# Optimization experiments

Hardware: AMD Instinct MI355X
Metric: run time of the kernel (lower is better)

The kernel has to match this reference:

```python
import jax, jax.numpy as jnp
import numpy as np

NUM_HEAD = 16
HIDDEN = 1024
HEAD_DIM = HIDDEN // NUM_HEAD


def setup_inputs() -> dict:
    key = jax.random.key(0)
    k1, k2, k3, k4, k5 = jax.random.split(key, 5)
    scale = 0.02
    x = jax.random.normal(k1, (2, 2048, HIDDEN), dtype=jnp.float32)
    w_in = jax.random.normal(k2, (3 * HIDDEN, HIDDEN), dtype=jnp.float32) * scale
    b_in = jax.random.normal(k3, (3 * HIDDEN,), dtype=jnp.float32) * scale
    w_out = jax.random.normal(k4, (HIDDEN, HIDDEN), dtype=jnp.float32) * scale
    b_out = jax.random.normal(k5, (HIDDEN,), dtype=jnp.float32) * scale
    return {"x": x, "w_in": w_in, "b_in": b_in, "w_out": w_out, "b_out": b_out}


def reference(x, w_in, b_in, w_out, b_out):
    B, S, D = x.shape
    # in_proj: fused QKV, torch Linear convention y = x @ W.T + b
    qkv = x @ w_in.T + b_in                      # [B,S,3D]
    q, k, v = jnp.split(qkv, 3, axis=-1)         # each [B,S,D]
    def heads(t):
        return t.reshape(B, S, NUM_HEAD, HEAD_DIM).transpose(0, 2, 1, 3)  # [B,H,S,d]
    q, k, v = heads(q), heads(k), heads(v)
    scores = jnp.einsum("bhqd,bhkd->bhqk", q, k) / jnp.sqrt(
        jnp.asarray(HEAD_DIM, dtype=x.dtype))    # [B,H,S,S]
    attn = jax.nn.softmax(scores, axis=-1)
    out = jnp.einsum("bhqk,bhkd->bhqd", attn, v)  # [B,H,S,d]
    out = out.transpose(0, 2, 1, 3).reshape(B, S, D)
    return out @ w_out.T + b_out
```

## Files before the change

kernel.cpp:

```cpp
#include <hip/hip_runtime.h>

using u16 = unsigned short;
using u32 = unsigned int;

typedef __bf16 bf16x8 __attribute__((ext_vector_type(8)));
typedef __bf16 bf16x2 __attribute__((ext_vector_type(2)));
typedef float f32x4 __attribute__((ext_vector_type(4)));

__device__ __forceinline__ u16 f2b(float x) {
  u32 u = __builtin_bit_cast(u32, x);
  u += 0x7fffu + ((u >> 16) & 1u);
  return (u16)(u >> 16);
}

__device__ __forceinline__ u32 pk2(float lo, float hi) {
  bf16x2 t;
  t[0] = (__bf16)lo;
  t[1] = (__bf16)hi;
  return __builtin_bit_cast(u32, t);
}

__device__ __forceinline__ void gload16(const u16* g, u16* l) {
  __builtin_amdgcn_global_load_lds(
      (const __attribute__((address_space(1))) void*)g,
      (__attribute__((address_space(3))) void*)l, 16, 0, 0);
}

#define SCALE_Q 0.1803368801111204f
#define DEFER_THR 8.0f

__global__ void cvt_bf16_k(const float* __restrict__ s, u16* __restrict__ d, int n8) {
  int i = blockIdx.x * blockDim.x + threadIdx.x;
  int stride = gridDim.x * blockDim.x;
  for (; i < n8; i += stride) {
    float4 a = ((const float4*)s)[2 * i];
    float4 b = ((const float4*)s)[2 * i + 1];
    uint4 o;
    o.x = (u32)f2b(a.x) | ((u32)f2b(a.y) << 16);
    o.y = (u32)f2b(a.z) | ((u32)f2b(a.w) << 16);
    o.z = (u32)f2b(b.x) | ((u32)f2b(b.y) << 16);
    o.w = (u32)f2b(b.z) | ((u32)f2b(b.w) << 16);
    ((uint4*)d)[i] = o;
  }
}

template <int MODE, int BM>
__global__ __launch_bounds__(256) void gemm_bt(
    const u16* __restrict__ A, const u16* __restrict__ Bm,
    const float* __restrict__ bias,
    u16* __restrict__ q, u16* __restrict__ k, u16* __restrict__ v,
    float* __restrict__ outf) {
  constexpr int KD = 1024;
  constexpr int MR = BM / 32;
  const int n0 = blockIdx.x * 128;
  const int m0 = blockIdx.y * BM;
  const int tid = threadIdx.x;
  const int wid = tid >> 6;
  const int lane = tid & 63;
  const int wr = wid >> 1, wc = wid & 1;
  const int fr = lane & 15, fg = lane >> 4;
  const int srow = lane >> 2;
  const int scol = (lane & 3) * 8;

  __shared__ __align__(16) u16 As[BM * 32];
  __shared__ __align__(16) u16 Bs[128 * 32];

  f32x4 acc[MR][4] = {};

  for (int k0 = 0; k0 < KD; k0 += 32) {
#pragma unroll
    for (int i = 0; i < BM / 64; ++i) {
      int row = i * 64 + wid * 16 + srow;
      gload16(A + (size_t)(m0 + row) * KD + k0 + scol, As + (i * 64 + wid * 16) * 32);
    }
#pragma unroll
    for (int i = 0; i < 2; ++i) {
      int row = i * 64 + wid * 16 + srow;
      gload16(Bm + (size_t)(n0 + row) * KD + k0 + scol, Bs + (i * 64 + wid * 16) * 32);
    }
    __syncthreads();
    bf16x8 af[MR], bfr[4];
#pragma unroll
    for (int r = 0; r < MR; ++r)
      af[r] = *(const bf16x8*)(As + (wr * (BM / 2) + r * 16 + fr) * 32 + fg * 8);
#pragma unroll
    for (int c = 0; c < 4; ++c)
      bfr[c] = *(const bf16x8*)(Bs + (wc * 64 + c * 16 + fr) * 32 + fg * 8);
#pragma unroll
    for (int r = 0; r < MR; ++r)
#pragma unroll
      for (int c = 0; c < 4; ++c)
        acc[r][c] = __builtin_amdgcn_mfma_f32_16x16x32_bf16(af[r], bfr[c], acc[r][c], 0, 0, 0);
    __syncthreads();
  }

#pragma unroll
  for (int r = 0; r < MR; ++r) {
#pragma unroll
    for (int c = 0; c < 4; ++c) {
      const int gcol = n0 + wc * 64 + c * 16 + fr;
      const float bv = bias[gcol];
#pragma unroll
      for (int g = 0; g < 4; ++g) {
        const int grow = m0 + wr * (BM / 2) + r * 16 + fg * 4 + g;
        float val = acc[r][c][g] + bv;
        if (MODE == 0) {
          const int which = gcol >> 10;
          if (which == 0) val *= SCALE_Q;
          const int dcol = gcol & 1023;
          const int hh = dcol >> 6, dd = dcol & 63;
          const int bb = grow >> 11, ss = grow & 2047;
          u16* dst = which == 0 ? q : (which == 1 ? k : v);
          dst[((size_t)((bb << 4) + hh) * 2048 + ss) * 64 + dd] = f2b(val);
        } else {
          outf[(size_t)grow * 1024 + gcol] = val;
        }
      }
    }
  }
}

__global__ __launch_bounds__(256) void attn_fwd(
    const u16* __restrict__ Q, const u16* __restrict__ K,
    const u16* __restrict__ V, u16* __restrict__ AO) {
  const int wg = blockIdx.x;
  const int newid = (wg & 7) * 64 + (wg >> 3);
  const int bh = newid >> 4;
  const int qt = newid & 15;
  const int b = bh >> 4, h = bh & 15;

  const int tid = threadIdx.x, wid = tid >> 6, lane = tid & 63;
  const int fr = lane & 15, fg = lane >> 4;
  const size_t base = (size_t)bh * (2048 * 64);
  const int q0 = qt * 128 + wid * 32;

  constexpr int LD = 72;
  __shared__ __align__(16) u16 Ks[2][64 * LD];
  __shared__ __align__(16) u16 Vs[2][64 * LD];

  bf16x8 qf[2][2];
#pragma unroll
  for (int rf = 0; rf < 2; ++rf)
#pragma unroll
    for (int ks = 0; ks < 2; ++ks)
      qf[rf][ks] = *(const bf16x8*)(Q + base + (size_t)(q0 + rf * 16 + fr) * 64 + ks * 32 + fg * 8);

  f32x4 o[2][4] = {};
  float mrow[2] = {-3.0e38f, -3.0e38f};
  float lrow[2] = {0.f, 0.f};

  const int krow = lane;
  const int Lrow = ((krow >> 5) << 5) | (((krow >> 3) & 1) << 4) | (((krow >> 2) & 1) << 3) |
                   (((krow >> 4) & 1) << 2) | (krow & 3);
  const int c0 = wid * 16;
  const int kp2 = (lane & 31) * 2;
  const int vh = (lane >> 5) * 8;

  uint4 kr0, kr1, vr0, vr1;
  {
    const u16* kp = K + base + (size_t)Lrow * 64 + c0;
    const u16* vp = V + base + (size_t)kp2 * 64 + c0 + vh;
    kr0 = *(const uint4*)kp; kr1 = *(const uint4*)(kp + 8);
    vr0 = *(const uint4*)vp; vr1 = *(const uint4*)(vp + 64);
  }

  for (int t = 0; t < 32; ++t) {
    u16* kb = (u16*)Ks[t & 1];
    u16* vb = (u16*)Vs[t & 1];
    *(uint4*)(kb + krow * LD + c0) = kr0;
    *(uint4*)(kb + krow * LD + c0 + 8) = kr1;
    {
      const u32* ra = (const u32*)&vr0;
      const u32* rb = (const u32*)&vr1;
#pragma unroll
      for (int j = 0; j < 8; ++j) {
        u32 w = __builtin_amdgcn_perm(rb[j >> 1], ra[j >> 1],
                                      (j & 1) ? 0x07060302u : 0x05040100u);
        *(u32*)(vb + (c0 + vh + j) * LD + kp2) = w;
      }
    }
    __syncthreads();
    if (t + 1 < 32) {
      const u16* kp = K + base + (size_t)((t + 1) * 64 + Lrow) * 64 + c0;
      const u16* vp = V + base + (size_t)((t + 1) * 64 + kp2) * 64 + c0 + vh;
      kr0 = *(const uint4*)kp; kr1 = *(const uint4*)(kp + 8);
      vr0 = *(const uint4*)vp; vr1 = *(const uint4*)(vp + 64);
    }

    bf16x8 kf[4][2], vf[4][2];
#pragma unroll
    for (int c = 0; c < 4; ++c)
#pragma unroll
      for (int ks = 0; ks < 2; ++ks)
        kf[c][ks] = *(const bf16x8*)(kb + (c * 16 + fr) * LD + ks * 32 + fg * 8);
#pragma unroll
    for (int d = 0; d < 4; ++d)
#pragma unroll
      for (int ks = 0; ks < 2; ++ks)
        vf[d][ks] = *(const bf16x8*)(vb + (d * 16 + fr) * LD + ks * 32 + fg * 8);

#pragma unroll
    for (int rf = 0; rf < 2; ++rf) {
      f32x4 p[4];
      __builtin_amdgcn_s_setprio(1);
#pragma unroll
      for (int c = 0; c < 4; ++c) {
        f32x4 z = {};
        z = __builtin_amdgcn_mfma_f32_16x16x32_bf16(kf[c][0], qf[rf][0], z, 0, 0, 0);
        z = __builtin_amdgcn_mfma_f32_16x16x32_bf16(kf[c][1], qf[rf][1], z, 0, 0, 0);
        p[c] = z;
      }
      __builtin_amdgcn_s_setprio(0);
      f32x4 m4 = p[0];
#pragma unroll
      for (int c = 1; c < 4; ++c) {
        m4[0] = fmaxf(m4[0], p[c][0]); m4[1] = fmaxf(m4[1], p[c][1]);
        m4[2] = fmaxf(m4[2], p[c][2]); m4[3] = fmaxf(m4[3], p[c][3]);
      }
      float mx = fmaxf(fmaxf(m4[0], m4[1]), fmaxf(m4[2], m4[3]));
      mx = fmaxf(mx, __shfl_xor(mx, 16));
      mx = fmaxf(mx, __shfl_xor(mx, 32));

      const float mold = mrow[rf];
      const bool defer = __all(mx <= mold + DEFER_THR);
      float mnew = mold, corr = 1.0f;
      if (!defer) {
        mnew = fmaxf(mold, mx);
        corr = __builtin_amdgcn_exp2f(mold - mnew);
        mrow[rf] = mnew;
      }
      float rs = 0.f;
#pragma unroll
      for (int c = 0; c < 4; ++c)
#pragma unroll
        for (int g = 0; g < 4; ++g) {
          const float pv = __builtin_amdgcn_exp2f(p[c][g] - mnew);
          p[c][g] = pv;
          rs += pv;
        }
      rs += __shfl_xor(rs, 16);
      rs += __shfl_xor(rs, 32);
      if (defer) {
        lrow[rf] += rs;
      } else {
        lrow[rf] = lrow[rf] * corr + rs;
        float cO[4];
#pragma unroll
        for (int g = 0; g < 4; ++g) cO[g] = __shfl(corr, 20 * fg + g);
#pragma unroll
        for (int d = 0; d < 4; ++d) {
          o[rf][d][0] *= cO[0]; o[rf][d][1] *= cO[1];
          o[rf][d][2] *= cO[2]; o[rf][d][3] *= cO[3];
        }
      }

      bf16x8 pa[2];
#pragma unroll
      for (int ks = 0; ks < 2; ++ks) {
        u32 w0 = pk2(p[2 * ks][0], p[2 * ks][1]);
        u32 w1 = pk2(p[2 * ks][2], p[2 * ks][3]);
        u32 w2 = pk2(p[2 * ks + 1][0], p[2 * ks + 1][1]);
        u32 w3 = pk2(p[2 * ks + 1][2], p[2 * ks + 1][3]);
        uint4 packed = {w0, w1, w2, w3};
        pa[ks] = __builtin_bit_cast(bf16x8, packed);
      }
      __builtin_amdgcn_s_setprio(1);
#pragma unroll
      for (int d = 0; d < 4; ++d) {
        o[rf][d] = __builtin_amdgcn_mfma_f32_16x16x32_bf16(pa[0], vf[d][0], o[rf][d], 0, 0, 0);
        o[rf][d] = __builtin_amdgcn_mfma_f32_16x16x32_bf16(pa[1], vf[d][1], o[rf][d], 0, 0, 0);
      }
      __builtin_amdgcn_s_setprio(0);
    }
  }

#pragma unroll
  for (int rf = 0; rf < 2; ++rf) {
    float rinv[4];
#pragma unroll
    for (int g = 0; g < 4; ++g)
      rinv[g] = __builtin_amdgcn_rcpf(__shfl(lrow[rf], 20 * fg + g));
#pragma unroll
    for (int d = 0; d < 4; ++d)
#pragma unroll
      for (int g = 0; g < 4; ++g) {
        const int qr = q0 + rf * 16 + fg * 4 + g;
        AO[(size_t)(b * 2048 + qr) * 1024 + h * 64 + d * 16 + fr] = f2b(o[rf][d][g] * rinv[g]);
      }
  }
}

extern "C" void kernel_launch(void* const* d_in, const int* in_sizes, int n_in,
                              void* d_out, int out_size, void* d_ws, size_t ws_size,
                              hipStream_t stream) {
  (void)in_sizes; (void)n_in; (void)out_size; (void)ws_size;
  const float* x     = (const float*)d_in[0];
  const float* w_in  = (const float*)d_in[1];
  const float* b_in  = (const float*)d_in[2];
  const float* w_out = (const float*)d_in[3];
  const float* b_out = (const float*)d_in[4];

  u16* xb    = (u16*)d_ws;
  u16* winb  = xb    + (size_t)4096 * 1024;
  u16* woutb = winb  + (size_t)3072 * 1024;
  u16* qb    = woutb + (size_t)1024 * 1024;
  u16* kb    = qb    + (size_t)4194304;
  u16* vb    = kb    + (size_t)4194304;
  u16* aob   = vb    + (size_t)4194304;

  cvt_bf16_k<<<2048, 256, 0, stream>>>(x, xb, 4096 * 1024 / 8);
  cvt_bf16_k<<<1536, 256, 0, stream>>>(w_in, winb, 3072 * 1024 / 8);
  cvt_bf16_k<<<512, 256, 0, stream>>>(w_out, woutb, 1024 * 1024 / 8);

  gemm_bt<0, 128><<<dim3(24, 32), 256, 0, stream>>>(xb, winb, b_in, qb, kb, vb, nullptr);
  attn_fwd<<<512, 256, 0, stream>>>(qb, kb, vb, aob);
  gemm_bt<1, 64><<<dim3(8, 64), 256, 0, stream>>>(aob, woutb, b_out, nullptr, nullptr, nullptr,
                                                  (float*)d_out);
}
```

Before: 199.0 us.

## Swizzle GEMM LDS tiles with K=64 steps and transpose attention PV accumulator layout

The projection GEMM now stages 64-wide K slices per iteration with an XOR-swizzled LDS layout. This halves the number of barriers and is meant to avoid LDS bank conflicts on fragment reads. In attention, the PV MFMA operands are swapped so each lane's output accumulator holds one query row. That removes the per-row correction and normalizer shuffles and allows packed 8-byte bf16 stores instead of scalar stores. The row max and sum reductions also use vector elementwise ops. The cost is more LDS per GEMM block, which may lower occupancy.

```diff
diff --git a/kernel.cpp b/kernel.cpp
--- a/kernel.cpp
+++ b/kernel.cpp
@@ -52,6 +52,7 @@
     float* __restrict__ outf) {
   constexpr int KD = 1024;
   constexpr int MR = BM / 32;
+  constexpr int CA = BM / 8;
   const int n0 = blockIdx.x * 128;
   const int m0 = blockIdx.y * BM;
   const int tid = threadIdx.x;
@@ -59,38 +60,45 @@
   const int lane = tid & 63;
   const int wr = wid >> 1, wc = wid & 1;
   const int fr = lane & 15, fg = lane >> 4;
-  const int srow = lane >> 2;
-  const int scol = (lane & 3) * 8;
-
-  __shared__ __align__(16) u16 As[BM * 32];
-  __shared__ __align__(16) u16 Bs[128 * 32];
+  const int srow = lane >> 3;
+  const int scol = ((lane & 7) ^ (srow & 7)) * 8;
+
+  __shared__ __align__(16) u16 As[BM * 64];
+  __shared__ __align__(16) u16 Bs[128 * 64];
 
   f32x4 acc[MR][4] = {};
 
-  for (int k0 = 0; k0 < KD; k0 += 32) {
-#pragma unroll
-    for (int i = 0; i < BM / 64; ++i) {
-      int row = i * 64 + wid * 16 + srow;
-      gload16(A + (size_t)(m0 + row) * KD + k0 + scol, As + (i * 64 + wid * 16) * 32);
-    }
-#pragma unroll
-    for (int i = 0; i < 2; ++i) {
-      int row = i * 64 + wid * 16 + srow;
-      gload16(Bm + (size_t)(n0 + row) * KD + k0 + scol, Bs + (i * 64 + wid * 16) * 32);
+  for (int k0 = 0; k0 < KD; k0 += 64) {
+#pragma unroll
+    for (int i = 0; i < CA / 4; ++i) {
+      const int chunk = wid * (CA / 4) + i;
+      gload16(A + (size_t)(m0 + chunk * 8 + srow) * KD + k0 + scol, As + chunk * 512);
+    }
+#pragma unroll
+    for (int i = 0; i < 4; ++i) {
+      const int chunk = wid * 4 + i;
+      gload16(Bm + (size_t)(n0 + chunk * 8 + srow) * KD + k0 + scol, Bs + chunk * 512);
     }
     __syncthreads();
-    bf16x8 af[MR], bfr[4];
-#pragma unroll
-    for (int r = 0; r < MR; ++r)
-      af[r] = *(const bf16x8*)(As + (wr * (BM / 2) + r * 16 + fr) * 32 + fg * 8);
-#pragma unroll
-    for (int c = 0; c < 4; ++c)
-      bfr[c] = *(const bf16x8*)(Bs + (wc * 64 + c * 16 + fr) * 32 + fg * 8);
-#pragma unroll
-    for (int r = 0; r < MR; ++r)
-#pragma unroll
-      for (int c = 0; c < 4; ++c)
-        acc[r][c] = __builtin_amdgcn_mfma_f32_16x16x32_bf16(af[r], bfr[c], acc[r][c], 0, 0, 0);
+#pragma unroll
+    for (int ks = 0; ks < 2; ++ks) {
+      bf16x8 af[MR], bfr[4];
+#pragma unroll
+      for (int r = 0; r < MR; ++r) {
+        const int row = wr * (BM / 2) + r * 16 + fr;
+        af[r] = *(const bf16x8*)(As + row * 64 + ((ks * 32 + fg * 8) ^ ((row & 7) * 8)));
+      }
+#pragma unroll
+      for (int c = 0; c < 4; ++c) {
+        const int row = wc * 64 + c * 16 + fr;
+        bfr[c] = *(const bf16x8*)(Bs + row * 64 + ((ks * 32 + fg * 8) ^ ((row & 7) * 8)));
+      }
+#pragma unroll
+      for (int r = 0; r < MR; ++r)
+#pragma unroll
+        for (int c = 0; c < 4; ++c)
+          acc[r][c] = __builtin_amdgcn_mfma_f32_16x16x32_bf16(af[r], bfr[c], acc[r][c], 0, 0, 0);
+    }
     __syncthreads();
   }
 
@@ -211,48 +219,34 @@
         p[c] = z;
       }
       __builtin_amdgcn_s_setprio(0);
-      f32x4 m4 = p[0];
-#pragma unroll
-      for (int c = 1; c < 4; ++c) {
-        m4[0] = fmaxf(m4[0], p[c][0]); m4[1] = fmaxf(m4[1], p[c][1]);
-        m4[2] = fmaxf(m4[2], p[c][2]); m4[3] = fmaxf(m4[3], p[c][3]);
-      }
+      f32x4 m01 = __builtin_elementwise_max(p[0], p[1]);
+      f32x4 m23 = __builtin_elementwise_max(p[2], p[3]);
+      f32x4 m4 = __builtin_elementwise_max(m01, m23);
       float mx = fmaxf(fmaxf(m4[0], m4[1]), fmaxf(m4[2], m4[3]));
       mx = fmaxf(mx, __shfl_xor(mx, 16));
       mx = fmaxf(mx, __shfl_xor(mx, 32));
 
       const float mold = mrow[rf];
       const bool defer = __all(mx <= mold + DEFER_THR);
-      float mnew = mold, corr = 1.0f;
+      float mnew = mold;
       if (!defer) {
         mnew = fmaxf(mold, mx);
-        corr = __builtin_amdgcn_exp2f(mold - mnew);
+        const float corr = __builtin_amdgcn_exp2f(mold - mnew);
         mrow[rf] = mnew;
-      }
-      float rs = 0.f;
+        lrow[rf] *= corr;
+#pragma unroll
+        for (int d = 0; d < 4; ++d) o[rf][d] *= corr;
+      }
 #pragma unroll
       for (int c = 0; c < 4; ++c)
 #pragma unroll
-        for (int g = 0; g < 4; ++g) {
-          const float pv = __builtin_amdgcn_exp2f(p[c][g] - mnew);
-          p[c][g] = pv;
-          rs += pv;
-        }
+        for (int g = 0; g < 4; ++g)
+          p[c][g] = __builtin_amdgcn_exp2f(p[c][g] - mnew);
+      f32x4 s4 = (p[0] + p[1]) + (p[2] + p[3]);
+      float rs = (s4[0] + s4[1]) + (s4[2] + s4[3]);
       rs += __shfl_xor(rs, 16);
       rs += __shfl_xor(rs, 32);
-      if (defer) {
-        lrow[rf] += rs;
-      } else {
-        lrow[rf] = lrow[rf] * corr + rs;
-        float cO[4];
-#pragma unroll
-        for (int g = 0; g < 4; ++g) cO[g] = __shfl(corr, 20 * fg + g);
-#pragma unroll
-        for (int d = 0; d < 4; ++d) {
-          o[rf][d][0] *= cO[0]; o[rf][d][1] *= cO[1];
-          o[rf][d][2] *= cO[2]; o[rf][d][3] *= cO[3];
-        }
-      }
+      lrow[rf] += rs;
 
       bf16x8 pa[2];
 #pragma unroll
@@ -267,8 +261,8 @@
       __builtin_amdgcn_s_setprio(1);
 #pragma unroll
       for (int d = 0; d < 4; ++d) {
-        o[rf][d] = __builtin_amdgcn_mfma_f32_16x16x32_bf16(pa[0], vf[d][0], o[rf][d], 0, 0, 0);
-        o[rf][d] = __builtin_amdgcn_mfma_f32_16x16x32_bf16(pa[1], vf[d][1], o[rf][d], 0, 0, 0);
+        o[rf][d] = __builtin_amdgcn_mfma_f32_16x16x32_bf16(vf[d][0], pa[0], o[rf][d], 0, 0, 0);
+        o[rf][d] = __builtin_amdgcn_mfma_f32_16x16x32_bf16(vf[d][1], pa[1], o[rf][d], 0, 0, 0);
       }
       __builtin_amdgcn_s_setprio(0);
     }
@@ -276,17 +270,15 @@
 
 #pragma unroll
   for (int rf = 0; rf < 2; ++rf) {
-    float rinv[4];
-#pragma unroll
-    for (int g = 0; g < 4; ++g)
-      rinv[g] = __builtin_amdgcn_rcpf(__shfl(lrow[rf], 20 * fg + g));
-#pragma unroll
-    for (int d = 0; d < 4; ++d)
-#pragma unroll
-      for (int g = 0; g < 4; ++g) {
-        const int qr = q0 + rf * 16 + fg * 4 + g;
-        AO[(size_t)(b * 2048 + qr) * 1024 + h * 64 + d * 16 + fr] = f2b(o[rf][d][g] * rinv[g]);
-      }
+    const float rinv = __builtin_amdgcn_rcpf(lrow[rf]);
+    const size_t rowoff = (size_t)(b * 2048 + q0 + rf * 16 + fr) * 1024 + h * 64;
+#pragma unroll
+    for (int d = 0; d < 4; ++d) {
+      uint2 st;
+      st.x = pk2(o[rf][d][0] * rinv, o[rf][d][1] * rinv);
+      st.y = pk2(o[rf][d][2] * rinv, o[rf][d][3] * rinv);
+      *(uint2*)(AO + rowoff + d * 16 + fg * 4) = st;
+    }
   }
 }
 
```

Measured after the change: 203.0 us. Within noise of the previous version (+2.0%).
